# Kernel optimization log

Hardware: AMD Instinct MI355X
Metric: run time of the kernel (lower is better)

The kernel has to match this reference:

```python
import jax, jax.numpy as jnp
import numpy as np

B, T, I, H = 256, 512, 300, 128


def setup_inputs() -> dict:
    key = jax.random.key(0)
    ks = jax.random.split(key, 7)
    s_ih = 1.0 / np.sqrt(H)
    return {
        "x": jax.random.normal(ks[0], (B, T, I), dtype=jnp.float32),
        # PyTorch LSTM params, gate order i,f,g,o stacked along first axis
        "W_ih": jax.random.uniform(ks[1], (4 * H, I), minval=-s_ih, maxval=s_ih, dtype=jnp.float32),
        "W_hh": jax.random.uniform(ks[2], (4 * H, H), minval=-s_ih, maxval=s_ih, dtype=jnp.float32),
        "b_ih": jax.random.uniform(ks[3], (4 * H,), minval=-s_ih, maxval=s_ih, dtype=jnp.float32),
        "b_hh": jax.random.uniform(ks[4], (4 * H,), minval=-s_ih, maxval=s_ih, dtype=jnp.float32),
        "fc_w": jax.random.uniform(ks[5], (1, H), minval=-s_ih, maxval=s_ih, dtype=jnp.float32),
        "fc_b": jax.random.uniform(ks[6], (1,), minval=-s_ih, maxval=s_ih, dtype=jnp.float32),
    }


def _lstm_last_h(x, W_ih, W_hh, b_ih, b_hh):
    # Precompute input contributions for all timesteps at once: [B,T,4H]
    xg = jnp.einsum("bti,gi->btg", x, W_ih) + b_ih + b_hh
    xg = jnp.transpose(xg, (1, 0, 2))  # [T,B,4H] for scan

    def step(carry, xg_t):
        h, c = carry
        gates = xg_t + h @ W_hh.T  # [B,4H]
        i, f, g, o = jnp.split(gates, 4, axis=-1)
        i = jax.nn.sigmoid(i)
        f = jax.nn.sigmoid(f)
        g = jnp.tanh(g)
        o = jax.nn.sigmoid(o)
        c = f * c + i * g
        h = o * jnp.tanh(c)
        return (h, c), None

    h0 = jnp.zeros((x.shape[0], W_hh.shape[1]), dtype=x.dtype)
    (h_last, _), _ = jax.lax.scan(step, (h0, h0), xg)
    return h_last  # [B,H]


def reference(x, W_ih, W_hh, b_ih, b_hh, fc_w, fc_b):
    h_last = _lstm_last_h(x, W_ih, W_hh, b_ih, b_hh)
    return h_last @ fc_w.T + fc_b  # [B,1]
```

## Files before the change

### kernel.cpp

```cpp
#include <hip/hip_runtime.h>
#include <cstdint>
#include <cstddef>

#define Bb   256
#define Tt   512
#define Ii   300
#define Hh   128
#define G4   512
#define KP   320
#define Mm   (Bb*Tt)

typedef _Float16 h2v   __attribute__((ext_vector_type(2)));
typedef _Float16 half8 __attribute__((ext_vector_type(8)));
typedef float    f32x4 __attribute__((ext_vector_type(4)));

static __device__ __forceinline__ h2v as_h2(unsigned int u){ union{unsigned int u; h2v h;} c; c.u=u; return c.h; }
static __device__ __forceinline__ unsigned int as_u32(h2v h){ union{unsigned int u; h2v h;} c; c.h=h; return c.u; }

#if __has_builtin(__builtin_amdgcn_fdot2)
#define FDOT2(a,b,c) __builtin_amdgcn_fdot2((a),(b),(c),false)
#else
static __device__ __forceinline__ float FDOT2(h2v a, h2v b, float c){
  return c + (float)a[0]*(float)b[0] + (float)a[1]*(float)b[1];
}
#endif

__global__ __launch_bounds__(256) void conv_x(const float* __restrict__ x, unsigned int* __restrict__ x16){
  int idx = blockIdx.x*256 + threadIdx.x;
  int r   = idx / 160;
  int kk2 = idx - r*160;
  int kk  = kk2*2;
  const float* xr = x + (size_t)r*Ii;
  float v0 = (kk   < Ii) ? xr[kk]   : 0.f;
  float v1 = (kk+1 < Ii) ? xr[kk+1] : 0.f;
  h2v h; h[0] = (_Float16)v0; h[1] = (_Float16)v1;
  x16[idx] = as_u32(h);
}

__global__ __launch_bounds__(256) void conv_small(const float* __restrict__ Wih, const float* __restrict__ Whh,
      const float* __restrict__ bih, const float* __restrict__ bhh,
      unsigned int* __restrict__ W16, unsigned int* __restrict__ Whh2, float* __restrict__ bias){
  int idx = blockIdx.x*256 + threadIdx.x;
  if (idx < G4*160){
    int r = idx/160, kk2 = idx - r*160, kk = kk2*2;
    const float* wr = Wih + (size_t)r*Ii;
    float v0 = (kk   < Ii) ? wr[kk]   : 0.f;
    float v1 = (kk+1 < Ii) ? wr[kk+1] : 0.f;
    h2v h; h[0]=(_Float16)v0; h[1]=(_Float16)v1;
    W16[idx] = as_u32(h);
  } else if (idx < G4*160 + G4*64){
    int t = idx - G4*160; int j = t>>6, kk = t&63;
    float v0 = Whh[j*Hh + kk*2], v1 = Whh[j*Hh + kk*2 + 1];
    h2v h; h[0]=(_Float16)v0; h[1]=(_Float16)v1;
    Whh2[t] = as_u32(h);
  } else if (idx < G4*160 + G4*64 + G4){
    int d = idx - (G4*160 + G4*64);
    bias[d] = bih[d] + bhh[d];
  }
}

__global__ __launch_bounds__(256,2) void gemm16(const _Float16* __restrict__ A, const _Float16* __restrict__ Bm,
       const float* __restrict__ bias, float* __restrict__ C){
  __shared__ _Float16 As[128][32];
  __shared__ _Float16 Bs[128][32];
  int tid = threadIdx.x;
  int w = tid>>6, lane = tid&63;
  int bm = blockIdx.x*128, bn = blockIdx.y*128;
  f32x4 acc[2][8];
  #pragma unroll
  for (int i=0;i<2;i++)
    #pragma unroll
    for (int j=0;j<8;j++) acc[i][j] = (f32x4){0.f,0.f,0.f,0.f};

  int srow = tid>>1, scol = (tid&1)*16;
  const uint4* ga = (const uint4*)(A  + (size_t)(bm+srow)*KP + scol);
  const uint4* gb = (const uint4*)(Bm + (size_t)(bn+srow)*KP + scol);

  int q = lane>>4, mr = lane&15;
  int m0 = w*32;

  for (int kt=0; kt<KP/32; ++kt){
    __syncthreads();
    uint4 va0 = ga[0], va1 = ga[1];
    uint4 vb0 = gb[0], vb1 = gb[1];
    *(uint4*)&As[srow][scol]   = va0; *(uint4*)&As[srow][scol+8] = va1;
    *(uint4*)&Bs[srow][scol]   = vb0; *(uint4*)&Bs[srow][scol+8] = vb1;
    ga += 4; gb += 4;
    __syncthreads();
    half8 af0 = *(const half8*)&As[m0 + mr][q*8];
    half8 af1 = *(const half8*)&As[m0 + 16 + mr][q*8];
    #pragma unroll
    for (int j=0;j<8;j++){
      half8 bf = *(const half8*)&Bs[j*16 + mr][q*8];
      acc[0][j] = __builtin_amdgcn_mfma_f32_16x16x32_f16(af0, bf, acc[0][j], 0,0,0);
      acc[1][j] = __builtin_amdgcn_mfma_f32_16x16x32_f16(af1, bf, acc[1][j], 0,0,0);
    }
  }
  #pragma unroll
  for (int j=0;j<8;j++){
    int gc = bn + j*16 + mr;
    float bv = bias[gc];
    #pragma unroll
    for (int i=0;i<2;i++){
      int gr0 = bm + w*32 + i*16 + q*4;
      #pragma unroll
      for (int reg=0; reg<4; ++reg)
        C[(size_t)(gr0+reg)*G4 + gc] = acc[i][j][reg] + bv;
    }
  }
}

__global__ __launch_bounds__(512,2) void lstm_rec(const float* __restrict__ xg, const unsigned int* __restrict__ Whh2,
     const float* __restrict__ fcw, const float* __restrict__ fcb, float* __restrict__ out){
  int tid = threadIdx.x;
  int b = blockIdx.x;
  int d = tid & 127, g = tid >> 7;
  h2v w[64];
  #pragma unroll
  for (int kk=0; kk<64; ++kk) w[kk] = as_h2(Whh2[tid*64 + kk]);

  __shared__ __align__(16) unsigned short hsh[128];
  __shared__ __align__(16) float gsh[512];
  __shared__ float red[128];
  if (tid < 128) hsh[tid] = 0;
  float creg = 0.f, hreg = 0.f;
  const float* xrow = xg + (size_t)b * (Tt*G4);
  float xc = xrow[tid];
  __syncthreads();

  for (int t=0; t<Tt; ++t){
    float xn = 0.f;
    if (t < Tt-1) xn = xrow[(size_t)(t+1)*G4 + tid];
    float a0 = xc, a1 = 0.f;
    const uint4* hv = (const uint4*)hsh;
    #pragma unroll
    for (int kq=0; kq<8; ++kq){
      uint4 hq0 = hv[kq*2], hq1 = hv[kq*2+1];
      a0 = FDOT2(as_h2(hq0.x), w[kq*8+0], a0); a1 = FDOT2(as_h2(hq0.y), w[kq*8+1], a1);
      a0 = FDOT2(as_h2(hq0.z), w[kq*8+2], a0); a1 = FDOT2(as_h2(hq0.w), w[kq*8+3], a1);
      a0 = FDOT2(as_h2(hq1.x), w[kq*8+4], a0); a1 = FDOT2(as_h2(hq1.y), w[kq*8+5], a1);
      a0 = FDOT2(as_h2(hq1.z), w[kq*8+6], a0); a1 = FDOT2(as_h2(hq1.w), w[kq*8+7], a1);
    }
    float a = a0 + a1;
    float act;
    if (g == 2){ float e = __expf(2.f*a); act = 1.f - 2.f/(e+1.f); }
    else       { act = 1.f/(1.f+__expf(-a)); }
    gsh[d*4+g] = act;
    __syncthreads();
    float4 gv = *(const float4*)&gsh[d*4];
    creg = gv.y*creg + gv.x*gv.z;
    float ec = __expf(2.f*creg); float tc = 1.f - 2.f/(ec+1.f);
    hreg = gv.w*tc;
    if (g == 0){
      union{ _Float16 f; unsigned short s; } cv; cv.f = (_Float16)hreg;
      hsh[d] = cv.s;
    }
    __syncthreads();
    xc = xn;
  }

  if (tid < 128) red[tid] = hreg * fcw[tid];
  __syncthreads();
  #pragma unroll
  for (int s=64; s>=1; s>>=1){
    if (tid < s) red[tid] += red[tid+s];
    __syncthreads();
  }
  if (tid == 0) out[b] = red[0] + fcb[0];
}

extern "C" void kernel_launch(void* const* d_in, const int* in_sizes, int n_in,
                              void* d_out, int out_size, void* d_ws, size_t ws_size,
                              hipStream_t stream){
  const float* x   = (const float*)d_in[0];
  const float* Wih = (const float*)d_in[1];
  const float* Whh = (const float*)d_in[2];
  const float* bih = (const float*)d_in[3];
  const float* bhh = (const float*)d_in[4];
  const float* fcw = (const float*)d_in[5];
  const float* fcb = (const float*)d_in[6];
  float* out = (float*)d_out;
  char* ws = (char*)d_ws;

  unsigned int* x16   = (unsigned int*)(ws);
  unsigned int* W16   = (unsigned int*)(ws + 83886080);
  unsigned int* Whh2w = (unsigned int*)(ws + 84213760);
  float*        bias  = (float*)      (ws + 84344832);
  float*        xg    = (float*)      (ws + 84346880);

  hipLaunchKernelGGL(conv_x,     dim3(81920),  dim3(256), 0, stream, x, x16);
  hipLaunchKernelGGL(conv_small, dim3(450),    dim3(256), 0, stream, Wih, Whh, bih, bhh, W16, Whh2w, bias);
  hipLaunchKernelGGL(gemm16,     dim3(1024,4), dim3(256), 0, stream,
                     (const _Float16*)x16, (const _Float16*)W16, bias, xg);
  hipLaunchKernelGGL(lstm_rec,   dim3(256),    dim3(512), 0, stream, xg, Whh2w, fcw, fcb, out);
}
```

Before: 661.8 us.

## Split LSTM gate dot products across thread pairs and use direct-to-LDS loads in GEMM

The recurrence kernel now uses 1024 threads per batch row. Each gate row's 128-length dot product is split across two lanes and combined with a shuffle, which halves the serial FDOT2 chain and the weight registers per thread. Gate activations are stored in gate-major shared memory. The input-projection GEMM now loads tiles with global_load_lds into XOR-swizzled LDS to avoid register staging and bank conflicts. In exchange, the larger blocks pay more for each __syncthreads, and the extra shuffle adds latency to every timestep.

```diff
diff --git a/kernel.cpp b/kernel.cpp
--- a/kernel.cpp
+++ b/kernel.cpp
@@ -8,11 +8,13 @@
 #define Hh   128
 #define G4   512
 #define KP   320
-#define Mm   (Bb*Tt)
 
 typedef _Float16 h2v   __attribute__((ext_vector_type(2)));
 typedef _Float16 half8 __attribute__((ext_vector_type(8)));
 typedef float    f32x4 __attribute__((ext_vector_type(4)));
+
+typedef __attribute__((address_space(3))) unsigned int lds_uint;
+typedef const __attribute__((address_space(1))) unsigned int glb_uint;
 
 static __device__ __forceinline__ h2v as_h2(unsigned int u){ union{unsigned int u; h2v h;} c; c.u=u; return c.h; }
 static __device__ __forceinline__ unsigned int as_u32(h2v h){ union{unsigned int u; h2v h;} c; c.h=h; return c.u; }
@@ -61,8 +63,8 @@
 
 __global__ __launch_bounds__(256,2) void gemm16(const _Float16* __restrict__ A, const _Float16* __restrict__ Bm,
        const float* __restrict__ bias, float* __restrict__ C){
-  __shared__ _Float16 As[128][32];
-  __shared__ _Float16 Bs[128][32];
+  __shared__ __align__(16) _Float16 As[128*32];
+  __shared__ __align__(16) _Float16 Bs[128*32];
   int tid = threadIdx.x;
   int w = tid>>6, lane = tid&63;
   int bm = blockIdx.x*128, bn = blockIdx.y*128;
@@ -72,26 +74,36 @@
     #pragma unroll
     for (int j=0;j<8;j++) acc[i][j] = (f32x4){0.f,0.f,0.f,0.f};
 
-  int srow = tid>>1, scol = (tid&1)*16;
-  const uint4* ga = (const uint4*)(A  + (size_t)(bm+srow)*KP + scol);
-  const uint4* gb = (const uint4*)(Bm + (size_t)(bn+srow)*KP + scol);
+  int L0 = w*128 + lane, L1 = L0 + 64;
+  int r0 = L0>>2, c0 = (L0&3) ^ (r0&3);
+  int r1 = L1>>2, c1 = (L1&3) ^ (r1&3);
+  const _Float16* gA0 = A  + (size_t)(bm+r0)*KP + c0*8;
+  const _Float16* gA1 = A  + (size_t)(bm+r1)*KP + c1*8;
+  const _Float16* gB0 = Bm + (size_t)(bn+r0)*KP + c0*8;
+  const _Float16* gB1 = Bm + (size_t)(bn+r1)*KP + c1*8;
 
   int q = lane>>4, mr = lane&15;
   int m0 = w*32;
+  int ra0 = m0+mr, ra1 = m0+16+mr;
+  int oa0 = ra0*32 + ((q ^ (ra0&3))*8);
+  int oa1 = ra1*32 + ((q ^ (ra1&3))*8);
+  int ob[8];
+  #pragma unroll
+  for (int j=0;j<8;j++){ int rb = j*16+mr; ob[j] = rb*32 + ((q ^ (rb&3))*8); }
 
   for (int kt=0; kt<KP/32; ++kt){
     __syncthreads();
-    uint4 va0 = ga[0], va1 = ga[1];
-    uint4 vb0 = gb[0], vb1 = gb[1];
-    *(uint4*)&As[srow][scol]   = va0; *(uint4*)&As[srow][scol+8] = va1;
-    *(uint4*)&Bs[srow][scol]   = vb0; *(uint4*)&Bs[srow][scol+8] = vb1;
-    ga += 4; gb += 4;
-    __syncthreads();
-    half8 af0 = *(const half8*)&As[m0 + mr][q*8];
-    half8 af1 = *(const half8*)&As[m0 + 16 + mr][q*8];
+    __builtin_amdgcn_global_load_lds((glb_uint*)gA0, (lds_uint*)&As[w*1024      ], 16, 0, 0);
+    __builtin_amdgcn_global_load_lds((glb_uint*)gA1, (lds_uint*)&As[w*1024 + 512], 16, 0, 0);
+    __builtin_amdgcn_global_load_lds((glb_uint*)gB0, (lds_uint*)&Bs[w*1024      ], 16, 0, 0);
+    __builtin_amdgcn_global_load_lds((glb_uint*)gB1, (lds_uint*)&Bs[w*1024 + 512], 16, 0, 0);
+    gA0 += 32; gA1 += 32; gB0 += 32; gB1 += 32;
+    __syncthreads();
+    half8 af0 = *(const half8*)&As[oa0];
+    half8 af1 = *(const half8*)&As[oa1];
     #pragma unroll
     for (int j=0;j<8;j++){
-      half8 bf = *(const half8*)&Bs[j*16 + mr][q*8];
+      half8 bf = *(const half8*)&Bs[ob[j]];
       acc[0][j] = __builtin_amdgcn_mfma_f32_16x16x32_f16(af0, bf, acc[0][j], 0,0,0);
       acc[1][j] = __builtin_amdgcn_mfma_f32_16x16x32_f16(af1, bf, acc[1][j], 0,0,0);
     }
@@ -110,60 +122,63 @@
   }
 }
 
-__global__ __launch_bounds__(512,2) void lstm_rec(const float* __restrict__ xg, const unsigned int* __restrict__ Whh2,
+__global__ __launch_bounds__(1024,4) void lstm_rec(const float* __restrict__ xg, const unsigned int* __restrict__ Whh2,
      const float* __restrict__ fcw, const float* __restrict__ fcb, float* __restrict__ out){
   int tid = threadIdx.x;
   int b = blockIdx.x;
-  int d = tid & 127, g = tid >> 7;
-  h2v w[64];
-  #pragma unroll
-  for (int kk=0; kk<64; ++kk) w[kk] = as_h2(Whh2[tid*64 + kk]);
+  int r = tid >> 1;
+  int s = tid & 1;
+  int d = r & 127;
+  h2v w[32];
+  #pragma unroll
+  for (int k=0; k<32; ++k) w[k] = as_h2(Whh2[r*64 + s*32 + k]);
 
   __shared__ __align__(16) unsigned short hsh[128];
-  __shared__ __align__(16) float gsh[512];
+  __shared__ float gsh[512];
   __shared__ float red[128];
   if (tid < 128) hsh[tid] = 0;
   float creg = 0.f, hreg = 0.f;
   const float* xrow = xg + (size_t)b * (Tt*G4);
-  float xc = xrow[tid];
+  float xc = xrow[r];
   __syncthreads();
 
   for (int t=0; t<Tt; ++t){
     float xn = 0.f;
-    if (t < Tt-1) xn = xrow[(size_t)(t+1)*G4 + tid];
-    float a0 = xc, a1 = 0.f;
-    const uint4* hv = (const uint4*)hsh;
+    if (t < Tt-1) xn = xrow[(size_t)(t+1)*G4 + r];
+    float a0 = (s==0) ? xc : 0.f, a1 = 0.f;
+    const uint4* hv = ((const uint4*)hsh) + s*8;
     #pragma unroll
     for (int kq=0; kq<8; ++kq){
-      uint4 hq0 = hv[kq*2], hq1 = hv[kq*2+1];
-      a0 = FDOT2(as_h2(hq0.x), w[kq*8+0], a0); a1 = FDOT2(as_h2(hq0.y), w[kq*8+1], a1);
-      a0 = FDOT2(as_h2(hq0.z), w[kq*8+2], a0); a1 = FDOT2(as_h2(hq0.w), w[kq*8+3], a1);
-      a0 = FDOT2(as_h2(hq1.x), w[kq*8+4], a0); a1 = FDOT2(as_h2(hq1.y), w[kq*8+5], a1);
-      a0 = FDOT2(as_h2(hq1.z), w[kq*8+6], a0); a1 = FDOT2(as_h2(hq1.w), w[kq*8+7], a1);
+      uint4 hq = hv[kq];
+      a0 = FDOT2(as_h2(hq.x), w[kq*4+0], a0);
+      a1 = FDOT2(as_h2(hq.y), w[kq*4+1], a1);
+      a0 = FDOT2(as_h2(hq.z), w[kq*4+2], a0);
+      a1 = FDOT2(as_h2(hq.w), w[kq*4+3], a1);
     }
     float a = a0 + a1;
+    a += __shfl_xor(a, 1, 64);
     float act;
-    if (g == 2){ float e = __expf(2.f*a); act = 1.f - 2.f/(e+1.f); }
-    else       { act = 1.f/(1.f+__expf(-a)); }
-    gsh[d*4+g] = act;
-    __syncthreads();
-    float4 gv = *(const float4*)&gsh[d*4];
-    creg = gv.y*creg + gv.x*gv.z;
+    if ((r >> 7) == 2){ float e = __expf(2.f*a); act = 1.f - 2.f/(e+1.f); }
+    else              { act = 1.f/(1.f+__expf(-a)); }
+    if (s == 0) gsh[r] = act;
+    __syncthreads();
+    float gi = gsh[d], gf = gsh[128+d], gg = gsh[256+d], go = gsh[384+d];
+    creg = gf*creg + gi*gg;
     float ec = __expf(2.f*creg); float tc = 1.f - 2.f/(ec+1.f);
-    hreg = gv.w*tc;
-    if (g == 0){
-      union{ _Float16 f; unsigned short s; } cv; cv.f = (_Float16)hreg;
-      hsh[d] = cv.s;
+    hreg = go*tc;
+    if (tid < 256 && s == 0){
+      union{ _Float16 f; unsigned short u; } cv; cv.f = (_Float16)hreg;
+      hsh[r] = cv.u;
     }
     __syncthreads();
     xc = xn;
   }
 
-  if (tid < 128) red[tid] = hreg * fcw[tid];
+  if (tid < 256 && s == 0) red[r] = hreg * fcw[r];
   __syncthreads();
   #pragma unroll
-  for (int s=64; s>=1; s>>=1){
-    if (tid < s) red[tid] += red[tid+s];
+  for (int st=64; st>=1; st>>=1){
+    if (tid < st) red[tid] += red[tid+st];
     __syncthreads();
   }
   if (tid == 0) out[b] = red[0] + fcb[0];
@@ -192,5 +207,5 @@
   hipLaunchKernelGGL(conv_small, dim3(450),    dim3(256), 0, stream, Wih, Whh, bih, bhh, W16, Whh2w, bias);
   hipLaunchKernelGGL(gemm16,     dim3(1024,4), dim3(256), 0, stream,
                      (const _Float16*)x16, (const _Float16*)W16, bias, xg);
-  hipLaunchKernelGGL(lstm_rec,   dim3(256),    dim3(512), 0, stream, xg, Whh2w, fcw, fcb, out);
-}
+  hipLaunchKernelGGL(lstm_rec,   dim3(256),    dim3(1024), 0, stream, xg, Whh2w, fcw, fcb, out);
+}
```

Result: slower. 732.4 us (+10.7%).
